# Performance work log

Measured on AMD Instinct MI355X. Metric: run time of the kernel, lower is better.

Reference implementation:

```python
import math
import jax, jax.numpy as jnp
import numpy as np
from jax import lax

B, T, D = 2, 2048, 1024
H, W, E = 16, 16, 8
HD = D // H


def setup_inputs() -> dict:
    key = jax.random.key(0)
    ks = jax.random.split(key, 9)
    s = 0.02
    return {
        "x": jax.random.normal(ks[0], (B, T, D), dtype=jnp.float32),
        # CausalConv1d weights: torch Conv1d layout [out_ch, in_ch, kernel]
        "q_w": jax.random.normal(ks[1], (D, D, W), dtype=jnp.float32) * s,
        "q_b": jax.random.normal(ks[2], (D,), dtype=jnp.float32) * s,
        "k_w": jax.random.normal(ks[3], (D, D, W), dtype=jnp.float32) * s,
        "k_b": jax.random.normal(ks[4], (D,), dtype=jnp.float32) * s,
        # Linear weights: torch layout [out, in]
        "v_w": jax.random.normal(ks[5], (D, D), dtype=jnp.float32) * s,
        "v_b": jax.random.normal(ks[6], (D,), dtype=jnp.float32) * s,
        "p_w": jax.random.normal(ks[7], (D, D), dtype=jnp.float32) * s,
        "p_b": jax.random.normal(ks[8], (D,), dtype=jnp.float32) * s,
    }


def _causal_conv(x_t, w, b):
    # x_t: [B, D, T]; left-pad by W-1 so output at t sees inputs <= t
    xp = jnp.pad(x_t, ((0, 0), (0, 0), (W - 1, 0)))
    y = lax.conv_general_dilated(xp, w, window_strides=(1,), padding="VALID",
                                 dimension_numbers=("NCH", "OIH", "NCH"))
    return y + b[None, :, None]


def _split_heads(z):
    # [B, T, D] -> [B, H, T, hd]
    return z.reshape(B, T, H, HD).transpose(0, 2, 1, 3)


def reference(x, q_w, q_b, k_w, k_b, v_w, v_b, p_w, p_b):
    x_t = x.transpose(0, 2, 1)  # [B, D, T]
    q = _split_heads(_causal_conv(x_t, q_w, q_b).transpose(0, 2, 1))
    k = _split_heads(_causal_conv(x_t, k_w, k_b).transpose(0, 2, 1))
    v = _split_heads(jnp.einsum("btd,od->bto", x, v_w) + v_b)
    scale = 1.0 / math.sqrt(HD)

    # ---- local window attention (unfold equivalent) ----
    # zero-pad keys/values W-1 steps to the left along T, gather sliding windows
    k_pad = jnp.pad(k, ((0, 0), (0, 0), (W - 1, 0), (0, 0)))
    v_pad = jnp.pad(v, ((0, 0), (0, 0), (W - 1, 0), (0, 0)))
    widx = jnp.arange(T)[:, None] + jnp.arange(W)[None, :]  # [T, W]
    patches_k = k_pad[:, :, widx]  # [B, H, T, W, hd]
    patches_v = v_pad[:, :, widx]  # [B, H, T, W, hd]
    attn_l = jax.nn.softmax(jnp.einsum("bhtd,bhtwd->bhtw", q, patches_k) * scale, axis=-1)
    out_l = jnp.einsum("bhtw,bhtwd->bhtd", attn_l, patches_v)

    # ---- exponential jumps: roll by 2^e (wrap-around, as in original) ----
    out_e = jnp.zeros_like(out_l)
    for e in range(E):
        shift = 2 ** e
        if shift >= T:
            break
        k_s = jnp.roll(k, -shift, axis=2)
        v_s = jnp.roll(v, -shift, axis=2)
        score = jnp.sum(q * k_s, axis=-1) * scale  # [B, H, T]
        alpha = jax.nn.softmax(score, axis=-1)[..., None]  # softmax over T (faithful)
        out_e = out_e + alpha * v_s

    out = (out_l + out_e).transpose(0, 2, 1, 3).reshape(B, T, D)
    return jnp.einsum("btd,od->bto", out, p_w) + p_b
```

## Files before the change

### kernel.cpp

```cpp
#include <hip/hip_runtime.h>
#include <cstdint>
#include <cstddef>

#define TSEQ 2048
#define DDIM 1024

typedef _Float16 f16;
typedef _Float16 f16x2 __attribute__((ext_vector_type(2)));
typedef _Float16 f16x4 __attribute__((ext_vector_type(4)));
typedef _Float16 f16x8 __attribute__((ext_vector_type(8)));
typedef float f32x4 __attribute__((ext_vector_type(4)));


__device__ __align__(16) static const unsigned char g_zero16[16] = {};

__device__ __forceinline__ void gload_lds16(const void* g, void* l) {
  __builtin_amdgcn_global_load_lds(
      (const __attribute__((address_space(1))) void*)g,
      (__attribute__((address_space(3))) void*)l, 16, 0, 0);
}

__global__ void cvt_all(const float* __restrict__ x, const float* __restrict__ vw,
                        const float* __restrict__ pw,
                        f16* __restrict__ xh, f16* __restrict__ vwh, f16* __restrict__ pwh) {
  int b = blockIdx.x;
  const float* src; f16* dst; int i;
  if (b < 4096)      { src = x;  dst = xh;  i = b * 256 + threadIdx.x; }
  else if (b < 5120) { src = vw; dst = vwh; i = (b - 4096) * 256 + threadIdx.x; }
  else               { src = pw; dst = pwh; i = (b - 5120) * 256 + threadIdx.x; }
  float4 v = ((const float4*)src)[i];
  f16x4 h = { (f16)v.x, (f16)v.y, (f16)v.z, (f16)v.w };
  ((f16x4*)dst)[i] = h;
}

__global__ __launch_bounds__(256) void cvt_w_tr(const float* __restrict__ qw,
                                                const float* __restrict__ kw,
                                                f16* __restrict__ qd, f16* __restrict__ kd) {
  __shared__ f16 tile[16][1032];
  const int o = blockIdx.x;
  const float* src; f16* dst;
  if (o < 1024) { src = qw + (size_t)o * 16384; dst = qd + (size_t)o * 16384; }
  else          { src = kw + (size_t)(o - 1024) * 16384; dst = kd + (size_t)(o - 1024) * 16384; }
  const int tid = threadIdx.x;
  #pragma unroll
  for (int p = 0; p < 16; p++) {
    const int idx = p * 256 + tid;
    const int i = idx >> 2, wq = idx & 3;
    float4 v = *(const float4*)(src + (size_t)i * 16 + wq * 4);
    tile[wq * 4 + 0][i] = (f16)v.x;
    tile[wq * 4 + 1][i] = (f16)v.y;
    tile[wq * 4 + 2][i] = (f16)v.z;
    tile[wq * 4 + 3][i] = (f16)v.w;
  }
  __syncthreads();
  #pragma unroll
  for (int p = 0; p < 8; p++) {
    const int c = p * 256 + tid;
    const int w = c >> 7, i8 = (c & 127) * 8;
    *(f16x8*)(dst + (size_t)w * 1024 + i8) = *(const f16x8*)&tile[w][i8];
  }
}

__global__ __launch_bounds__(256, 2) void gemm_qk(
    const f16* __restrict__ xh,
    const f16* __restrict__ Bq, const f16* __restrict__ Bk,
    const float* __restrict__ bq, const float* __restrict__ bk,
    f16* __restrict__ oq, f16* __restrict__ ok)
{
  __shared__ __align__(16) f16 smem[32768];
  const int tid = threadIdx.x;
  const int lane = tid & 63;
  const int wid = tid >> 6;
  const int wm = wid & 1;
  const int ks = wid >> 1;

  const int m0 = blockIdx.x * 128;
  const int n0 = blockIdx.y * 64;
  const int bT = m0 & ~(TSEQ - 1);
  const int t0 = m0 & (TSEQ - 1);

  const int srow = lane >> 3;
  const int scg = ((lane & 7) ^ ((lane >> 3) & 7)) * 8;

  f32x4 accq[4][4] = {};
  f32x4 acck[4][4] = {};

  const int slotoff = (((ks * 4 + (lane >> 4)) ^ (lane & 7)) * 8);

  auto stage = [&](int kk, int buf) {
    f16* sb = &smem[buf * 16384];
    if (wid < 2) {
      const int w = kk >> 10;
      const int i0 = (kk & (DDIM - 1)) + scg;
      #pragma unroll
      for (int c = 0; c < 8; c++) {
        const int s = wid * 8 + c;
        const int r = s * 8 + srow;
        const int srcT = t0 + r + w - 15;
        const void* g = (srcT >= 0)
            ? (const void*)(xh + (((size_t)(bT + srcT)) << 10) + i0)
            : (const void*)g_zero16;
        gload_lds16(g, (void*)&sb[s * 512]);
      }
    } else if (wid == 2) {
      #pragma unroll
      for (int c = 0; c < 8; c++) {
        const int r = c * 8 + srow;
        const void* g = (const void*)(Bq + ((size_t)(n0 + r) << 14) + kk + scg);
        gload_lds16(g, (void*)&sb[8192 + c * 512]);
      }
    } else {
      #pragma unroll
      for (int c = 0; c < 8; c++) {
        const int r = c * 8 + srow;
        const void* g = (const void*)(Bk + ((size_t)(n0 + r) << 14) + kk + scg);
        gload_lds16(g, (void*)&sb[12288 + c * 512]);
      }
    }
  };

  stage(0, 0);
  for (int kk = 0; kk < 16384; kk += 64) {
    const int buf = (kk >> 6) & 1;
    __syncthreads();
    if (kk + 64 < 16384) stage(kk + 64, buf ^ 1);

    const f16* sb = &smem[buf * 16384];
    f16x8 af[4], bfq[4], bfk[4];
    #pragma unroll
    for (int i = 0; i < 4; i++) {
      const int r = wm * 64 + i * 16 + (lane & 15);
      af[i] = *(const f16x8*)&sb[r * 64 + slotoff];
    }
    #pragma unroll
    for (int j = 0; j < 4; j++) {
      const int r = j * 16 + (lane & 15);
      bfq[j] = *(const f16x8*)&sb[8192 + r * 64 + slotoff];
      bfk[j] = *(const f16x8*)&sb[12288 + r * 64 + slotoff];
    }
    #pragma unroll
    for (int i = 0; i < 4; i++)
      #pragma unroll
      for (int j = 0; j < 4; j++) {
        accq[i][j] = __builtin_amdgcn_mfma_f32_16x16x32_f16(af[i], bfq[j], accq[i][j], 0, 0, 0);
        acck[i][j] = __builtin_amdgcn_mfma_f32_16x16x32_f16(af[i], bfk[j], acck[i][j], 0, 0, 0);
      }
  }

  const int crow = (lane >> 4) * 4;
  const int ccol = lane & 15;
  const int hh = n0 >> 6;
  float* red = (float*)smem + wm * 4096;

  __syncthreads();
  if (ks == 1) {
    #pragma unroll
    for (int i = 0; i < 4; i++)
      #pragma unroll
      for (int j = 0; j < 4; j++)
        #pragma unroll
        for (int r = 0; r < 4; r++)
          red[(i * 16 + crow + r) * 64 + j * 16 + ccol] = accq[i][j][r];
  }
  __syncthreads();
  if (ks == 0) {
    #pragma unroll
    for (int j = 0; j < 4; j++) {
      const int col = n0 + j * 16 + ccol;
      const float bvl = bq[col];
      const int d = j * 16 + ccol;
      #pragma unroll
      for (int i = 0; i < 4; i++)
        #pragma unroll
        for (int r = 0; r < 4; r++) {
          const int row = m0 + wm * 64 + i * 16 + crow + r;
          const int b = row >> 11, t = row & (TSEQ - 1);
          const float v = accq[i][j][r] + red[(i * 16 + crow + r) * 64 + j * 16 + ccol] + bvl;
          oq[((size_t)(b * 16 + hh) * TSEQ + t) * 64 + d] = (f16)v;
        }
    }
  }
  __syncthreads();
  if (ks == 1) {
    #pragma unroll
    for (int i = 0; i < 4; i++)
      #pragma unroll
      for (int j = 0; j < 4; j++)
        #pragma unroll
        for (int r = 0; r < 4; r++)
          red[(i * 16 + crow + r) * 64 + j * 16 + ccol] = acck[i][j][r];
  }
  __syncthreads();
  if (ks == 0) {
    #pragma unroll
    for (int j = 0; j < 4; j++) {
      const int col = n0 + j * 16 + ccol;
      const float bvl = bk[col];
      const int d = j * 16 + ccol;
      #pragma unroll
      for (int i = 0; i < 4; i++)
        #pragma unroll
        for (int r = 0; r < 4; r++) {
          const int row = m0 + wm * 64 + i * 16 + crow + r;
          const int b = row >> 11, t = row & (TSEQ - 1);
          const float v = acck[i][j][r] + red[(i * 16 + crow + r) * 64 + j * 16 + ccol] + bvl;
          ok[((size_t)(b * 16 + hh) * TSEQ + t) * 64 + d] = (f16)v;
        }
    }
  }
}

template<int MODE>
__global__ __launch_bounds__(256, 2) void gemm_small(
    const f16* __restrict__ A, const f16* __restrict__ Bw,
    const float* __restrict__ bias, f16* __restrict__ oh, float* __restrict__ ofp)
{
  __shared__ f16 As[128 * 32];
  __shared__ f16 Bs[128 * 32];
  const int tid = threadIdx.x;
  const int lane = tid & 63;
  const int wid = tid >> 6;
  const int m0 = blockIdx.x * 128;
  const int n0 = blockIdx.y * 128;

  const int srow = lane >> 2;
  const int scg = ((lane & 3) ^ ((lane >> 3) & 3)) * 8;
  const int wm = wid & 1;
  const int wn = wid >> 1;

  f32x4 acc[4][4] = {};

  for (int kk = 0; kk < 1024; kk += 32) {
    __syncthreads();
    if (wid < 2) {
      #pragma unroll
      for (int c = 0; c < 4; c++) {
        const int r = wid * 64 + c * 16 + srow;
        const void* g = (const void*)(A + (((size_t)(m0 + r)) << 10) + kk + scg);
        gload_lds16(g, (void*)&As[(wid * 64 + c * 16) * 32]);
      }
    } else {
      #pragma unroll
      for (int c = 0; c < 4; c++) {
        const int r = (wid - 2) * 64 + c * 16 + srow;
        const void* g = (const void*)(Bw + (((size_t)(n0 + r)) << 10) + kk + scg);
        gload_lds16(g, (void*)&Bs[((wid - 2) * 64 + c * 16) * 32]);
      }
    }
    __syncthreads();
    const int koff = ((lane >> 4) ^ ((lane >> 1) & 3)) * 8;
    f16x8 af[4], bf[4];
    #pragma unroll
    for (int i = 0; i < 4; i++) {
      af[i] = *(const f16x8*)&As[(wm * 64 + i * 16 + (lane & 15)) * 32 + koff];
      bf[i] = *(const f16x8*)&Bs[(wn * 64 + i * 16 + (lane & 15)) * 32 + koff];
    }
    #pragma unroll
    for (int i = 0; i < 4; i++)
      #pragma unroll
      for (int j = 0; j < 4; j++)
        acc[i][j] = __builtin_amdgcn_mfma_f32_16x16x32_f16(af[i], bf[j], acc[i][j], 0, 0, 0);
  }

  const int crow = (lane >> 4) * 4;
  const int ccol = lane & 15;
  #pragma unroll
  for (int j = 0; j < 4; j++) {
    const int col = n0 + wn * 64 + j * 16 + ccol;
    const float bvl = bias[col];
    #pragma unroll
    for (int i = 0; i < 4; i++) {
      #pragma unroll
      for (int r = 0; r < 4; r++) {
        const int row = m0 + wm * 64 + i * 16 + crow + r;
        const float val = acc[i][j][r] + bvl;
        if (MODE == 1) {
          ofp[(size_t)row * DDIM + col] = val;
        } else {
          const int b = row >> 11, t = row & (TSEQ - 1);
          const int h = col >> 6, d = col & 63;
          oh[((size_t)(b * 16 + h) * TSEQ + t) * 64 + d] = (f16)val;
        }
      }
    }
  }
}

__global__ __launch_bounds__(256) void score_k(const f16* __restrict__ qh,
                                               const f16* __restrict__ kh,
                                               float* __restrict__ scores) {
  const int bid = blockIdx.x;
  const int bh = bid >> 5, tc = bid & 31;
  const int tid = threadIdx.x;
  const int wave = tid >> 6, lane = tid & 63;
  const int tr = lane >> 3, dc = lane & 7;
  const size_t base = ((size_t)bh) << 17;
  const f16* qb = qh + base;
  const f16* kb = kh + base;

  #pragma unroll
  for (int p = 0; p < 2; p++) {
    const int t = tc * 64 + p * 32 + wave * 8 + tr;
    f16x8 qv = *(const f16x8*)(qb + (size_t)t * 64 + dc * 8);
    const f16x2* qp = (const f16x2*)&qv;
    #pragma unroll
    for (int e = 0; e < 8; e++) {
      const int ts = (t + (1 << e)) & (TSEQ - 1);
      f16x8 kv = *(const f16x8*)(kb + (size_t)ts * 64 + dc * 8);
      const f16x2* kp = (const f16x2*)&kv;
      float s = 0.f;
      #pragma unroll
      for (int j = 0; j < 4; j++) s = __builtin_amdgcn_fdot2(qp[j], kp[j], s, false);
      s += __shfl_xor(s, 1, 64);
      s += __shfl_xor(s, 2, 64);
      s += __shfl_xor(s, 4, 64);
      if (dc == 0) scores[((size_t)(bh * 8 + e) << 11) + t] = s * 0.125f;
    }
  }
}

__global__ void softmax_k(float* __restrict__ scores) {
  __shared__ float red[4];
  int row = blockIdx.x;
  float* p = scores + ((size_t)row << 11);
  int tid = threadIdx.x;
  float v[8];
  float4 a = ((const float4*)p)[tid * 2];
  float4 b = ((const float4*)p)[tid * 2 + 1];
  v[0] = a.x; v[1] = a.y; v[2] = a.z; v[3] = a.w;
  v[4] = b.x; v[5] = b.y; v[6] = b.z; v[7] = b.w;
  float m = v[0];
  #pragma unroll
  for (int j = 1; j < 8; j++) m = fmaxf(m, v[j]);
  for (int o = 32; o > 0; o >>= 1) m = fmaxf(m, __shfl_xor(m, o, 64));
  if ((tid & 63) == 0) red[tid >> 6] = m;
  __syncthreads();
  m = fmaxf(fmaxf(red[0], red[1]), fmaxf(red[2], red[3]));
  __syncthreads();
  float s = 0.f;
  #pragma unroll
  for (int j = 0; j < 8; j++) { v[j] = __expf(v[j] - m); s += v[j]; }
  for (int o = 32; o > 0; o >>= 1) s += __shfl_xor(s, o, 64);
  if ((tid & 63) == 0) red[tid >> 6] = s;
  __syncthreads();
  s = (red[0] + red[1]) + (red[2] + red[3]);
  float inv = 1.0f / s;
  float4 o1 = make_float4(v[0] * inv, v[1] * inv, v[2] * inv, v[3] * inv);
  float4 o2 = make_float4(v[4] * inv, v[5] * inv, v[6] * inv, v[7] * inv);
  ((float4*)p)[tid * 2] = o1;
  ((float4*)p)[tid * 2 + 1] = o2;
}

__global__ __launch_bounds__(256) void attn_out_k(
    const f16* __restrict__ qh, const f16* __restrict__ kh, const f16* __restrict__ vh,
    const float* __restrict__ alpha, f16* __restrict__ outh)
{
  __shared__ f16 qL[64 * 64];
  __shared__ f16 kL[80 * 64];
  __shared__ f16 vL[208 * 64];
  __shared__ float scL[64 * 16];
  __shared__ float aL[8 * 64];
  const int bh = blockIdx.x, tc = blockIdx.y;
  const int t0 = tc * 64;
  const int tid = threadIdx.x;
  const size_t base = ((size_t)bh) << 17;

  for (int idx = tid; idx < 64 * 8; idx += 256) {
    int r = idx >> 3, c = idx & 7, sl = c ^ (r & 7);
    *(uint4*)&qL[r * 64 + sl * 8] = *(const uint4*)(qh + base + (size_t)(t0 + r) * 64 + c * 8);
  }
  for (int idx = tid; idx < 79 * 8; idx += 256) {
    int r = idx >> 3, c = idx & 7, sl = c ^ (r & 7);
    int g = t0 - 15 + r;
    uint4 val = (g < 0) ? make_uint4(0, 0, 0, 0)
                        : *(const uint4*)(kh + base + (size_t)g * 64 + c * 8);
    *(uint4*)&kL[r * 64 + sl * 8] = val;
  }
  for (int idx = tid; idx < 207 * 8; idx += 256) {
    int r = idx >> 3, c = idx & 7, sl = c ^ (r & 7);
    int g = t0 - 15 + r;
    uint4 val;
    if (g < 0) val = make_uint4(0, 0, 0, 0);
    else {
      if (g >= TSEQ) g -= TSEQ;
      val = *(const uint4*)(vh + base + (size_t)g * 64 + c * 8);
    }
    *(uint4*)&vL[r * 64 + sl * 8] = val;
  }
  for (int idx = tid; idx < 512; idx += 256) {
    int e = idx >> 6, i = idx & 63;
    aL[e * 64 + i] = alpha[((size_t)(bh * 8 + e) << 11) + t0 + i];
  }
  __syncthreads();

  {
    const int tl = tid & 63;
    const int wg = tid >> 6;
    f16x8 qv[8];
    #pragma unroll
    for (int c = 0; c < 8; c++) qv[c] = *(const f16x8*)&qL[tl * 64 + ((c ^ (tl & 7)) * 8)];
    const f16x2* qp = (const f16x2*)&qv[0];
    #pragma unroll
    for (int wi = 0; wi < 4; wi++) {
      const int w = wg * 4 + wi;
      const int r = tl + w;
      float s = 0.f;
      #pragma unroll
      for (int c = 0; c < 8; c++) {
        f16x8 kv = *(const f16x8*)&kL[r * 64 + ((c ^ (r & 7)) * 8)];
        const f16x2* kp = (const f16x2*)&kv;
        #pragma unroll
        for (int j = 0; j < 4; j++) s = __builtin_amdgcn_fdot2(qp[c * 4 + j], kp[j], s, false);
      }
      scL[tl * 16 + w] = s * 0.125f;
    }
  }
  __syncthreads();

  if (tid < 64) {
    float sc[16];
    float m = -1e30f;
    #pragma unroll
    for (int w = 0; w < 16; w++) { sc[w] = scL[tid * 16 + w]; m = fmaxf(m, sc[w]); }
    float sum = 0.f;
    #pragma unroll
    for (int w = 0; w < 16; w++) { sc[w] = __expf(sc[w] - m); sum += sc[w]; }
    float inv = 1.0f / sum;
    #pragma unroll
    for (int w = 0; w < 16; w++) scL[tid * 16 + w] = sc[w] * inv;
  }
  __syncthreads();

  {
    const int tl = tid >> 2;
    const int qd = tid & 3;
    float accv[16] = {};
    #pragma unroll
    for (int w = 0; w < 16; w++) {
      const float pw_ = scL[tl * 16 + w];
      const int r = tl + w;
      #pragma unroll
      for (int c2 = 0; c2 < 2; c2++) {
        const int c = qd * 2 + c2;
        f16x8 v = *(const f16x8*)&vL[r * 64 + ((c ^ (r & 7)) * 8)];
        #pragma unroll
        for (int j = 0; j < 8; j++) accv[c2 * 8 + j] += pw_ * (float)v[j];
      }
    }
    #pragma unroll
    for (int e = 0; e < 8; e++) {
      const float a = aL[e * 64 + tl];
      const int r = tl + 15 + (1 << e);
      #pragma unroll
      for (int c2 = 0; c2 < 2; c2++) {
        const int c = qd * 2 + c2;
        f16x8 v = *(const f16x8*)&vL[r * 64 + ((c ^ (r & 7)) * 8)];
        #pragma unroll
        for (int j = 0; j < 8; j++) accv[c2 * 8 + j] += a * (float)v[j];
      }
    }
    const int b = bh >> 4, h = bh & 15;
    f16* orow = outh + ((size_t)(b * TSEQ + t0 + tl)) * DDIM + h * 64 + qd * 16;
    #pragma unroll
    for (int c2 = 0; c2 < 2; c2++) {
      f16x8 v;
      #pragma unroll
      for (int j = 0; j < 8; j++) v[j] = (f16)accv[c2 * 8 + j];
      *(f16x8*)(orow + c2 * 8) = v;
    }
  }
}

extern "C" void kernel_launch(void* const* d_in, const int* in_sizes, int n_in,
                              void* d_out, int out_size, void* d_ws, size_t ws_size,
                              hipStream_t stream) {
  (void)in_sizes; (void)n_in; (void)out_size; (void)ws_size;
  const float* x   = (const float*)d_in[0];
  const float* q_w = (const float*)d_in[1];
  const float* q_b = (const float*)d_in[2];
  const float* k_w = (const float*)d_in[3];
  const float* k_b = (const float*)d_in[4];
  const float* v_w = (const float*)d_in[5];
  const float* v_b = (const float*)d_in[6];
  const float* p_w = (const float*)d_in[7];
  const float* p_b = (const float*)d_in[8];
  float* out = (float*)d_out;

  char* ws = (char*)d_ws;
  f16* xh      = (f16*)(ws);
  f16* qwh     = (f16*)(ws + 8388608);
  f16* kwh     = (f16*)(ws + 41943040);
  f16* vwh     = (f16*)(ws + 75497472);
  f16* pwh     = (f16*)(ws + 77594624);
  f16* qh      = (f16*)(ws + 79691776);
  f16* kh      = (f16*)(ws + 88080384);
  f16* vh      = (f16*)(ws + 96468992);
  f16* outh    = (f16*)(ws + 104857600);
  float* alpha = (float*)(ws + 113246208);

  cvt_all<<<6144, 256, 0, stream>>>(x, v_w, p_w, xh, vwh, pwh);
  cvt_w_tr<<<2048, 256, 0, stream>>>(q_w, k_w, qwh, kwh);

  gemm_qk<<<dim3(32, 16), 256, 0, stream>>>(xh, qwh, kwh, q_b, k_b, qh, kh);
  gemm_small<0><<<dim3(32, 8), 256, 0, stream>>>(xh, vwh, v_b, vh, nullptr);

  score_k<<<1024, 256, 0, stream>>>(qh, kh, alpha);
  softmax_k<<<256, 256, 0, stream>>>(alpha);
  attn_out_k<<<dim3(32, 32), 256, 0, stream>>>(qh, kh, vh, alpha, outh);

  gemm_small<1><<<dim3(32, 8), 256, 0, stream>>>(outh, pwh, p_b, nullptr, out);
}
```

Measured before the change: 534.7 us.

## Rewrite Q/K conv GEMM as 8-wave triple-buffered pipeline without split-K reduction

The fused Q/K convolution GEMM now uses 512-thread blocks covering 256 rows. Each wave computes either Q or K for 64 rows over the full K dimension, which removes the split-K LDS reduction epilogue. A three-stage dynamic-shared-memory ring (144KB) replaces the double buffer. Loads are issued between half-tile MFMA phases with explicit vmcnt waits, raw s_barrier and setprio, to overlap global-to-LDS traffic with compute. This halves the grid to 256 blocks at one block per CU, which risks lower occupancy and fewer blocks than CUs.

```diff
diff --git a/kernel.cpp b/kernel.cpp
--- a/kernel.cpp
+++ b/kernel.cpp
@@ -61,151 +61,141 @@
   }
 }
 
-__global__ __launch_bounds__(256, 2) void gemm_qk(
+__global__ __launch_bounds__(512, 1) void gemm_qk8(
     const f16* __restrict__ xh,
     const f16* __restrict__ Bq, const f16* __restrict__ Bk,
     const float* __restrict__ bq, const float* __restrict__ bk,
     f16* __restrict__ oq, f16* __restrict__ ok)
 {
-  __shared__ __align__(16) f16 smem[32768];
+  extern __shared__ __align__(16) f16 smem[];
   const int tid = threadIdx.x;
   const int lane = tid & 63;
   const int wid = tid >> 6;
-  const int wm = wid & 1;
-  const int ks = wid >> 1;
-
-  const int m0 = blockIdx.x * 128;
+  const int wq = wid >> 1;
+  const int wp = wid & 1;
+
+  const int m0 = blockIdx.x * 256;
   const int n0 = blockIdx.y * 64;
   const int bT = m0 & ~(TSEQ - 1);
   const int t0 = m0 & (TSEQ - 1);
 
   const int srow = lane >> 3;
-  const int scg = ((lane & 7) ^ ((lane >> 3) & 7)) * 8;
-
-  f32x4 accq[4][4] = {};
-  f32x4 acck[4][4] = {};
-
-  const int slotoff = (((ks * 4 + (lane >> 4)) ^ (lane & 7)) * 8);
-
-  auto stage = [&](int kk, int buf) {
-    f16* sb = &smem[buf * 16384];
-    if (wid < 2) {
-      const int w = kk >> 10;
-      const int i0 = (kk & (DDIM - 1)) + scg;
-      #pragma unroll
-      for (int c = 0; c < 8; c++) {
-        const int s = wid * 8 + c;
-        const int r = s * 8 + srow;
-        const int srcT = t0 + r + w - 15;
-        const void* g = (srcT >= 0)
-            ? (const void*)(xh + (((size_t)(bT + srcT)) << 10) + i0)
-            : (const void*)g_zero16;
-        gload_lds16(g, (void*)&sb[s * 512]);
-      }
-    } else if (wid == 2) {
-      #pragma unroll
-      for (int c = 0; c < 8; c++) {
-        const int r = c * 8 + srow;
-        const void* g = (const void*)(Bq + ((size_t)(n0 + r) << 14) + kk + scg);
-        gload_lds16(g, (void*)&sb[8192 + c * 512]);
-      }
+  const int chunk8 = (((lane & 7) ^ (srow & 7)) << 3);
+
+  f32x4 acc[4][4] = {};
+
+  auto stageA = [&](int kt, int buf) {
+    const int kk = kt << 6;
+    const int w = kk >> 10;
+    const int i0 = kk & (DDIM - 1);
+    f16* sb = smem + buf * 24576;
+    #pragma unroll
+    for (int c = 0; c < 4; c++) {
+      const int rr = wid * 32 + c * 8;
+      const int srcT = t0 + rr + srow + w - 15;
+      const void* g = (srcT >= 0)
+          ? (const void*)(xh + (((size_t)(bT + srcT)) << 10) + i0 + chunk8)
+          : (const void*)g_zero16;
+      gload_lds16(g, (void*)&sb[rr * 64]);
+    }
+  };
+  auto stageB = [&](int kt, int buf) {
+    const int kk = kt << 6;
+    f16* sb = smem + buf * 24576 + (wid < 4 ? 16384 : 20480);
+    const f16* Bsrc = (wid < 4) ? Bq : Bk;
+    const int wb = wid & 3;
+    #pragma unroll
+    for (int c = 0; c < 2; c++) {
+      const int rr = wb * 16 + c * 8;
+      const void* g = (const void*)(Bsrc + (((size_t)(n0 + rr + srow)) << 14) + kk + chunk8);
+      gload_lds16(g, (void*)&sb[rr * 64]);
+    }
+  };
+
+  stageA(0, 0); stageB(0, 0);
+  stageA(1, 1); stageB(1, 1);
+
+  const int NT = 16384 / 64;
+  int buf = 0;
+  for (int kt = 0; kt < NT; kt++) {
+    if (kt < NT - 1) {
+      asm volatile("s_waitcnt vmcnt(6)" ::: "memory");
     } else {
-      #pragma unroll
-      for (int c = 0; c < 8; c++) {
-        const int r = c * 8 + srow;
-        const void* g = (const void*)(Bk + ((size_t)(n0 + r) << 14) + kk + scg);
-        gload_lds16(g, (void*)&sb[12288 + c * 512]);
-      }
-    }
-  };
-
-  stage(0, 0);
-  for (int kk = 0; kk < 16384; kk += 64) {
-    const int buf = (kk >> 6) & 1;
-    __syncthreads();
-    if (kk + 64 < 16384) stage(kk + 64, buf ^ 1);
-
-    const f16* sb = &smem[buf * 16384];
-    f16x8 af[4], bfq[4], bfk[4];
-    #pragma unroll
-    for (int i = 0; i < 4; i++) {
-      const int r = wm * 64 + i * 16 + (lane & 15);
-      af[i] = *(const f16x8*)&sb[r * 64 + slotoff];
-    }
-    #pragma unroll
-    for (int j = 0; j < 4; j++) {
-      const int r = j * 16 + (lane & 15);
-      bfq[j] = *(const f16x8*)&sb[8192 + r * 64 + slotoff];
-      bfk[j] = *(const f16x8*)&sb[12288 + r * 64 + slotoff];
-    }
-    #pragma unroll
-    for (int i = 0; i < 4; i++)
-      #pragma unroll
-      for (int j = 0; j < 4; j++) {
-        accq[i][j] = __builtin_amdgcn_mfma_f32_16x16x32_f16(af[i], bfq[j], accq[i][j], 0, 0, 0);
-        acck[i][j] = __builtin_amdgcn_mfma_f32_16x16x32_f16(af[i], bfk[j], acck[i][j], 0, 0, 0);
-      }
-  }
-
-  const int crow = (lane >> 4) * 4;
+      asm volatile("s_waitcnt vmcnt(0)" ::: "memory");
+    }
+    __builtin_amdgcn_s_barrier();
+    __builtin_amdgcn_sched_barrier(0);
+
+    const f16* sb = smem + buf * 24576;
+    const f16* bsb = sb + (wp ? 20480 : 16384);
+    const int stq = kt + 2;
+    const int sbuf = (buf >= 1) ? buf - 1 : 2;
+
+    {
+      const int slot = (((lane >> 4)) ^ (lane & 7)) << 3;
+      f16x8 af[4], bf[4];
+      #pragma unroll
+      for (int i = 0; i < 4; i++)
+        af[i] = *(const f16x8*)&sb[(wq * 64 + i * 16 + (lane & 15)) * 64 + slot];
+      #pragma unroll
+      for (int j = 0; j < 4; j++)
+        bf[j] = *(const f16x8*)&bsb[(j * 16 + (lane & 15)) * 64 + slot];
+      if (stq < NT) stageA(stq, sbuf);
+      __builtin_amdgcn_s_barrier();
+      asm volatile("s_waitcnt lgkmcnt(0)" ::: "memory");
+      __builtin_amdgcn_sched_barrier(0);
+      __builtin_amdgcn_s_setprio(1);
+      #pragma unroll
+      for (int i = 0; i < 4; i++)
+        #pragma unroll
+        for (int j = 0; j < 4; j++)
+          acc[i][j] = __builtin_amdgcn_mfma_f32_16x16x32_f16(af[i], bf[j], acc[i][j], 0, 0, 0);
+      __builtin_amdgcn_s_setprio(0);
+    }
+
+    {
+      const int slot = ((4 + (lane >> 4)) ^ (lane & 7)) << 3;
+      f16x8 af[4], bf[4];
+      #pragma unroll
+      for (int i = 0; i < 4; i++)
+        af[i] = *(const f16x8*)&sb[(wq * 64 + i * 16 + (lane & 15)) * 64 + slot];
+      #pragma unroll
+      for (int j = 0; j < 4; j++)
+        bf[j] = *(const f16x8*)&bsb[(j * 16 + (lane & 15)) * 64 + slot];
+      if (stq < NT) stageB(stq, sbuf);
+      __builtin_amdgcn_s_barrier();
+      asm volatile("s_waitcnt lgkmcnt(0)" ::: "memory");
+      __builtin_amdgcn_sched_barrier(0);
+      __builtin_amdgcn_s_setprio(1);
+      #pragma unroll
+      for (int i = 0; i < 4; i++)
+        #pragma unroll
+        for (int j = 0; j < 4; j++)
+          acc[i][j] = __builtin_amdgcn_mfma_f32_16x16x32_f16(af[i], bf[j], acc[i][j], 0, 0, 0);
+      __builtin_amdgcn_s_setprio(0);
+    }
+
+    buf = (buf == 2) ? 0 : buf + 1;
+  }
+
+  const int crow = (lane >> 4) << 2;
   const int ccol = lane & 15;
   const int hh = n0 >> 6;
-  float* red = (float*)smem + wm * 4096;
-
-  __syncthreads();
-  if (ks == 1) {
-    #pragma unroll
-    for (int i = 0; i < 4; i++)
-      #pragma unroll
-      for (int j = 0; j < 4; j++)
-        #pragma unroll
-        for (int r = 0; r < 4; r++)
-          red[(i * 16 + crow + r) * 64 + j * 16 + ccol] = accq[i][j][r];
-  }
-  __syncthreads();
-  if (ks == 0) {
-    #pragma unroll
-    for (int j = 0; j < 4; j++) {
-      const int col = n0 + j * 16 + ccol;
-      const float bvl = bq[col];
-      const int d = j * 16 + ccol;
-      #pragma unroll
-      for (int i = 0; i < 4; i++)
-        #pragma unroll
-        for (int r = 0; r < 4; r++) {
-          const int row = m0 + wm * 64 + i * 16 + crow + r;
-          const int b = row >> 11, t = row & (TSEQ - 1);
-          const float v = accq[i][j][r] + red[(i * 16 + crow + r) * 64 + j * 16 + ccol] + bvl;
-          oq[((size_t)(b * 16 + hh) * TSEQ + t) * 64 + d] = (f16)v;
-        }
-    }
-  }
-  __syncthreads();
-  if (ks == 1) {
-    #pragma unroll
-    for (int i = 0; i < 4; i++)
-      #pragma unroll
-      for (int j = 0; j < 4; j++)
-        #pragma unroll
-        for (int r = 0; r < 4; r++)
-          red[(i * 16 + crow + r) * 64 + j * 16 + ccol] = acck[i][j][r];
-  }
-  __syncthreads();
-  if (ks == 0) {
-    #pragma unroll
-    for (int j = 0; j < 4; j++) {
-      const int col = n0 + j * 16 + ccol;
-      const float bvl = bk[col];
-      const int d = j * 16 + ccol;
-      #pragma unroll
-      for (int i = 0; i < 4; i++)
-        #pragma unroll
-        for (int r = 0; r < 4; r++) {
-          const int row = m0 + wm * 64 + i * 16 + crow + r;
-          const int b = row >> 11, t = row & (TSEQ - 1);
-          const float v = acck[i][j][r] + red[(i * 16 + crow + r) * 64 + j * 16 + ccol] + bvl;
-          ok[((size_t)(b * 16 + hh) * TSEQ + t) * 64 + d] = (f16)v;
-        }
+  const float* bias = wp ? bk : bq;
+  f16* outp = wp ? ok : oq;
+  #pragma unroll
+  for (int j = 0; j < 4; j++) {
+    const int col = n0 + j * 16 + ccol;
+    const float bvl = bias[col];
+    const int d = (j << 4) + ccol;
+    #pragma unroll
+    for (int i = 0; i < 4; i++) {
+      #pragma unroll
+      for (int r = 0; r < 4; r++) {
+        const int row = m0 + wq * 64 + i * 16 + crow + r;
+        const int b = row >> 11, t = row & (TSEQ - 1);
+        outp[((size_t)(b * 16 + hh) * TSEQ + t) * 64 + d] = (f16)(acc[i][j][r] + bvl);
+      }
     }
   }
 }
@@ -498,10 +488,17 @@
   f16* outh    = (f16*)(ws + 104857600);
   float* alpha = (float*)(ws + 113246208);
 
+  static int s_attr_done = 0;
+  if (!s_attr_done) {
+    hipFuncSetAttribute((const void*)gemm_qk8,
+                        hipFuncAttributeMaxDynamicSharedMemorySize, 147456);
+    s_attr_done = 1;
+  }
+
   cvt_all<<<6144, 256, 0, stream>>>(x, v_w, p_w, xh, vwh, pwh);
   cvt_w_tr<<<2048, 256, 0, stream>>>(q_w, k_w, qwh, kwh);
 
-  gemm_qk<<<dim3(32, 16), 256, 0, stream>>>(xh, qwh, kwh, q_b, k_b, qh, kh);
+  gemm_qk8<<<dim3(16, 16), 512, 147456, stream>>>(xh, qwh, kwh, q_b, k_b, qh, kh);
   gemm_small<0><<<dim3(32, 8), 256, 0, stream>>>(xh, vwh, v_b, vh, nullptr);
 
   score_k<<<1024, 256, 0, stream>>>(qh, kh, alpha);
```

Result: faster. 517.3 us (-3.3%).
